# Kernel optimization log

Hardware: AMD Instinct MI355X
Metric: run time of the kernel (lower is better)

Reference implementation:

```python
import jax, jax.numpy as jnp
import numpy as np

WS = 7            # cubic window
HEADS = 6
DIM = 96          # attention channel dim (concat of two half-streams)
CH = 48           # per-stream channels (dim // 2)
HID = 384         # int(dim * mlp_ratio)
N = WS ** 3       # 343 tokens per window
EPS = 1e-5


def _rel_pos_index():
    c = np.stack(np.meshgrid(np.arange(WS), np.arange(WS), np.arange(WS), indexing='ij')).reshape(3, -1)
    rel = (c[:, :, None] - c[:, None, :]).transpose(1, 2, 0) + (WS - 1)
    rel[:, :, 0] *= (2 * WS - 1) * (2 * WS - 1)
    rel[:, :, 1] *= (2 * WS - 1)
    return rel.sum(-1)  # (N, N) int

RPI = jnp.asarray(_rel_pos_index())


def _ln(x, g, b):
    m = x.mean(-1, keepdims=True)
    v = ((x - m) ** 2).mean(-1, keepdims=True)
    return (x - m) * jax.lax.rsqrt(v + EPS) * g + b


def _win_part(x):
    B, H, W, T, C = x.shape
    x = x.reshape(B, H // WS, WS, W // WS, WS, T // WS, WS, C)
    return x.transpose(0, 1, 3, 5, 2, 4, 6, 7).reshape(-1, WS, WS, WS, C)


def _win_rev(w, B, H, W, T):
    C = w.shape[-1]
    x = w.reshape(B, H // WS, W // WS, T // WS, WS, WS, WS, C)
    return x.transpose(0, 1, 4, 2, 5, 3, 6, 7).reshape(B, H, W, T, C)


def _chessboard(wa, wb, gd, gh, gw):
    C = wa.shape[-1]
    a = wa.reshape(gd, gh, gw, WS, WS, WS, C)
    b = wb.reshape(gd, gh, gw, WS, WS, WS, C)
    i = jnp.arange(gd)[:, None, None]
    j = jnp.arange(gh)[None, :, None]
    k = jnp.arange(gw)[None, None, :]
    m = (((i + j + k) % 2) == 0)[..., None, None, None, None]
    return (jnp.where(m, a, b).reshape(-1, WS, WS, WS, C),
            jnp.where(m, b, a).reshape(-1, WS, WS, WS, C))


def _attn(x, mask, rpb, qkv_w, qkv_b, proj_w, proj_b):
    B_, n, C = x.shape
    hd = C // HEADS
    qkv = (x @ qkv_w + qkv_b).reshape(B_, n, 3, HEADS, hd).transpose(2, 0, 3, 1, 4)
    q, k, v = qkv[0] * (hd ** -0.5), qkv[1], qkv[2]
    att = jnp.einsum('bhnd,bhmd->bhnm', q, k)
    att = att + rpb[RPI].transpose(2, 0, 1)[None]   # relative position bias gather
    att = att + mask[:, None]                        # shift mask; B_ == nW since B == 1
    att = jax.nn.softmax(att, axis=-1)
    out = jnp.einsum('bhnm,bhmd->bhnd', att, v).transpose(0, 2, 1, 3).reshape(B_, n, C)
    return out @ proj_w + proj_b


def _mlp(x, w1, b1, w2, b2):
    return jax.nn.gelu(x @ w1 + b1, approximate=False) @ w2 + b2


def _forward(x_a, x_b, mask_matrix, n1a_g, n1a_b, n1b_g, n1b_b,
             rpb_a, qkvw_a, qkvb_a, projw_a, projb_a,
             rpb_b, qkvw_b, qkvb_b, projw_b, projb_b,
             n2a_g, n2a_b, n2b_g, n2b_b,
             fc1w_a, fc1b_a, fc2w_a, fc2b_a, fc1w_b, fc1b_b, fc2w_b, fc2b_b,
             gw1, gw2, gb2, H, W, T):
    B, L, _ = x_a.shape
    sa0, sb0 = x_a, x_b
    a = _ln(x_a, n1a_g, n1a_b).reshape(B, H, W, T, CH)
    b = _ln(x_b, n1b_g, n1b_b).reshape(B, H, W, T, CH)
    # chessboard cross-stream shuffle of windows (shifted-window branch)
    ca, cb = _chessboard(_win_part(a), _win_part(b), H // WS, W // WS, T // WS)
    a_cr = _win_rev(ca, B, H, W, T)
    b_cr = _win_rev(cb, B, H, W, T)
    neg, pos, dims = (-3, -3, -3), (3, 3, 3), (1, 2, 3)
    sa, sb = jnp.roll(a, neg, dims), jnp.roll(b, neg, dims)
    sac, sbc = jnp.roll(a_cr, neg, dims), jnp.roll(b_cr, neg, dims)
    xa_w = _win_part(jnp.concatenate([sa, sbc], -1)).reshape(-1, N, DIM)
    xb_w = _win_part(jnp.concatenate([sb, sac], -1)).reshape(-1, N, DIM)
    oa = _attn(xa_w, mask_matrix, rpb_a, qkvw_a, qkvb_a, projw_a, projb_a)
    ob = _attn(xb_w, mask_matrix, rpb_b, qkvw_b, qkvb_b, projw_b, projb_b)
    oa = jnp.roll(_win_rev(oa.reshape(-1, WS, WS, WS, DIM), B, H, W, T), pos, dims)[..., :CH].reshape(B, L, CH)
    ob = jnp.roll(_win_rev(ob.reshape(-1, WS, WS, WS, DIM), B, H, W, T), pos, dims)[..., :CH].reshape(B, L, CH)
    x_a = sa0 + oa
    x_b = sb0 + ob
    x_a = x_a + _mlp(_ln(x_a, n2a_g, n2a_b), fc1w_a, fc1b_a, fc2w_a, fc2b_a)
    x_b = x_b + _mlp(_ln(x_b, n2b_g, n2b_b), fc1w_b, fc1b_b, fc2w_b, fc2b_b)
    g = jax.nn.sigmoid(jnp.maximum(x_a.mean(1) @ gw1, 0.0) @ gw2 + gb2)[:, :, None]  # (B,1,1)
    x_a = x_a + g * x_b
    return x_a, x_b


def setup_inputs():
    key = jax.random.key(0)
    ks = iter(jax.random.split(key, 24))
    H = W = T = 35
    L = H * W * T
    nW = (H // WS) * (W // WS) * (T // WS)
    p = lambda shape: jax.random.normal(next(ks), shape, jnp.float32) * 0.02
    d = {
        'x_a': jax.random.normal(next(ks), (1, L, CH), jnp.float32),
        'x_b': jax.random.normal(next(ks), (1, L, CH), jnp.float32),
        'mask_matrix': jax.random.normal(next(ks), (nW, N, N), jnp.float32),
        'n1a_g': jnp.ones((CH,), jnp.float32), 'n1a_b': jnp.zeros((CH,), jnp.float32),
        'n1b_g': jnp.ones((CH,), jnp.float32), 'n1b_b': jnp.zeros((CH,), jnp.float32),
        'rpb_a': p(((2 * WS - 1) ** 3, HEADS)),
        'qkvw_a': p((DIM, 3 * DIM)), 'qkvb_a': jnp.zeros((3 * DIM,), jnp.float32),
        'projw_a': p((DIM, DIM)), 'projb_a': jnp.zeros((DIM,), jnp.float32),
        'rpb_b': p(((2 * WS - 1) ** 3, HEADS)),
        'qkvw_b': p((DIM, 3 * DIM)), 'qkvb_b': jnp.zeros((3 * DIM,), jnp.float32),
        'projw_b': p((DIM, DIM)), 'projb_b': jnp.zeros((DIM,), jnp.float32),
        'n2a_g': jnp.ones((CH,), jnp.float32), 'n2a_b': jnp.zeros((CH,), jnp.float32),
        'n2b_g': jnp.ones((CH,), jnp.float32), 'n2b_b': jnp.zeros((CH,), jnp.float32),
        'fc1w_a': p((CH, HID)), 'fc1b_a': jnp.zeros((HID,), jnp.float32),
        'fc2w_a': p((HID, CH)), 'fc2b_a': jnp.zeros((CH,), jnp.float32),
        'fc1w_b': p((CH, HID)), 'fc1b_b': jnp.zeros((HID,), jnp.float32),
        'fc2w_b': p((HID, CH)), 'fc2b_b': jnp.zeros((CH,), jnp.float32),
        'gw1': p((CH, CH // 4)), 'gw2': p((CH // 4, 1)),
        'gb2': jnp.full((1,), -2.0, jnp.float32),
        'H': H, 'W': W, 'T': T,
    }
    return d


def reference(x_a, x_b, mask_matrix, n1a_g, n1a_b, n1b_g, n1b_b,
              rpb_a, qkvw_a, qkvb_a, projw_a, projb_a,
              rpb_b, qkvw_b, qkvb_b, projw_b, projb_b,
              n2a_g, n2a_b, n2b_g, n2b_b,
              fc1w_a, fc1b_a, fc2w_a, fc2b_a, fc1w_b, fc1b_b, fc2w_b, fc2b_b,
              gw1, gw2, gb2, H, W, T):
    return _forward(x_a, x_b, mask_matrix, n1a_g, n1a_b, n1b_g, n1b_b,
                    rpb_a, qkvw_a, qkvb_a, projw_a, projb_a,
                    rpb_b, qkvw_b, qkvb_b, projw_b, projb_b,
                    n2a_g, n2a_b, n2b_g, n2b_b,
                    fc1w_a, fc1b_a, fc2w_a, fc2b_a, fc1w_b, fc1b_b, fc2w_b, fc2b_b,
                    gw1, gw2, gb2, H, W, T)
```

## Files before the change

### kernel.cpp

```cpp
#include <hip/hip_runtime.h>
#include <hip/hip_fp16.h>

#define LQ    42875
#define NTOK  343
#define X1SZ  2058000

#define OFF_MEAN 0
#define OFF_QKV  36928
#define OFF_WF   12500000
#define OFF_RPB  12600000
#define QKV_BYTES_NEEDED 56100000ull

typedef _Float16 f16x8 __attribute__((ext_vector_type(8)));
typedef float f32x4 __attribute__((ext_vector_type(4)));
union B128 { uint4 u; f16x8 h; _Float16 e[8]; };

__device__ __forceinline__ int src_index(int w, int i, int& par) {
  int gi = w / 25, gj = (w / 5) % 5, gk = w % 5;
  int ph = i / 49, pw = (i / 7) % 7, pt = i % 7;
  int hs = gi * 7 + ph + 3; if (hs >= 35) hs -= 35;
  int wd = gj * 7 + pw + 3; if (wd >= 35) wd -= 35;
  int td = gk * 7 + pt + 3; if (td >= 35) td -= 35;
  par = ((hs / 7) + (wd / 7) + (td / 7)) & 1;
  return (hs * 35 + wd) * 35 + td;
}

__global__ __launch_bounds__(64) void k_init(float* __restrict__ ws) {
  if (threadIdx.x < 49) ws[threadIdx.x] = 0.f;
}

__global__ __launch_bounds__(256) void k_pack(
    const float* __restrict__ w1a, const float* __restrict__ w1b,
    const float* __restrict__ w2a, const float* __restrict__ w2b,
    const float* __restrict__ qwa, const float* __restrict__ qwb,
    float* __restrict__ ws) {
  int idx = blockIdx.x * 256 + threadIdx.x;
  if (idx >= 17664) return;
  uint4* WFB = (uint4*)(ws + OFF_WF);
  unsigned short h[8];
  uint4* dst;
  if (idx < 10752) {
    int s = idx / 5376, r = idx - s * 5376;
    uint4* WF = WFB + (size_t)s * 5376;
    if (r < 3072) {
      int jn = r / 128, t = r - jn * 128, kk = t / 64, lane = t - kk * 64;
      int q = lane >> 4, n = lane & 15;
      const float* w1 = s ? w1b : w1a;
      int j = jn * 16 + n;
#pragma unroll
      for (int e = 0; e < 8; e++) {
        int k = kk * 32 + q * 8 + e;
        float v = (k < 48) ? w1[k * 384 + j] : 0.f;
        h[e] = __half_as_ushort(__float2half(v));
      }
    } else {
      int rr = r - 3072;
      int kt = rr / 192, t = rr - kt * 192, cn = t / 64, lane = t - cn * 64;
      int q = lane >> 4, n = lane & 15;
      const float* w2 = s ? w2b : w2a;
      int c = cn * 16 + n;
#pragma unroll
      for (int e = 0; e < 8; e++) {
        int j = kt * 32 + q * 8 + e;
        h[e] = __half_as_ushort(__float2half(w2[j * 48 + c]));
      }
    }
    dst = WF + r;
  } else {
    int idx2 = idx - 10752;
    int s = idx2 / 3456, r = idx2 - s * 3456;
    int jn = r / 192, t = r - jn * 192, kk = t / 64, lane = t - kk * 64;
    int q = lane >> 4, n = lane & 15;
    const float* qw = s ? qwb : qwa;
    int j = jn * 16 + n;
#pragma unroll
    for (int e = 0; e < 8; e++) {
      int k = kk * 32 + q * 8 + e;
      h[e] = __half_as_ushort(__float2half(qw[k * 288 + j]));
    }
    dst = WFB + 10752 + (size_t)s * 3456 + r;
  }
  uint4 u;
  u.x = (unsigned)h[0] | ((unsigned)h[1] << 16);
  u.y = (unsigned)h[2] | ((unsigned)h[3] << 16);
  u.z = (unsigned)h[4] | ((unsigned)h[5] << 16);
  u.w = (unsigned)h[6] | ((unsigned)h[7] << 16);
  *dst = u;
}

__global__ __launch_bounds__(256) void k_rpb(
    const float* __restrict__ rpa, const float* __restrict__ rpbp,
    float* __restrict__ ws) {
  int sh = blockIdx.y;
  int s = sh / 6, h = sh - s * 6;
  int idx = blockIdx.x * 256 + threadIdx.x;
  if (idx >= 117649) return;
  int ir = idx / 343, j = idx - ir * 343;
  int bi = (ir / 49) * 169 + ((ir / 7) % 7) * 13 + (ir % 7) + 1098;
  int bj = (j / 49) * 169 + ((j / 7) % 7) * 13 + (j % 7);
  const float* rp = s ? rpbp : rpa;
  ws[OFF_RPB + (size_t)sh * 117649 + idx] = rp[(bi - bj) * 6 + h];
}

__global__ __launch_bounds__(256) void k_qkv(
    const float* __restrict__ xa, const float* __restrict__ xb,
    const float* __restrict__ ga, const float* __restrict__ ba,
    const float* __restrict__ gb, const float* __restrict__ bb,
    const float* __restrict__ qba, const float* __restrict__ qbb,
    const float* __restrict__ ws, __half* __restrict__ qkvh) {
  __shared__ uint4 LDSB[2368];
  int s = blockIdx.z;
  int tid = threadIdx.x;
  int wid = tid >> 6, lane = tid & 63;
  int quad = lane >> 4, n15 = lane & 15;
  uint4* WR = LDSB + wid * 592;
  _Float16* th = (_Float16*)WR;
  int tbase = blockIdx.x * 64 + wid * 16;

  if (lane < 32) {
    int tt = lane & 15, which = lane >> 4;
    int t = tbase + tt;
    float v[48];
    bool wr = false, dup = false;
    if (t < LQ) {
      int w = t / 343, i = t - w * 343;
      int par; int src = src_index(w, i, par);
      const float* xr; const float* G; const float* B;
      bool doit;
      if (which == 0) { xr = (s ? xb : xa) + src * 48; G = s ? gb : ga; B = s ? bb : ba; doit = true; dup = (par == 1); }
      else            { xr = (s ? xa : xb) + src * 48; G = s ? ga : gb; B = s ? ba : bb; doit = (par == 0); }
      if (doit) {
        float sm = 0.f, sq = 0.f;
#pragma unroll
        for (int q4 = 0; q4 < 12; q4++) {
          float4 tv = ((const float4*)xr)[q4];
          v[4 * q4] = tv.x; v[4 * q4 + 1] = tv.y; v[4 * q4 + 2] = tv.z; v[4 * q4 + 3] = tv.w;
          sm += tv.x + tv.y + tv.z + tv.w;
          sq += tv.x * tv.x + tv.y * tv.y + tv.z * tv.z + tv.w * tv.w;
        }
        float m = sm * (1.f / 48.f);
        float r = rsqrtf(sq * (1.f / 48.f) - m * m + 1e-5f);
#pragma unroll
        for (int k = 0; k < 48; k++) v[k] = (v[k] - m) * r * G[k] + B[k];
        wr = true;
      }
    } else if (which == 0) {
#pragma unroll
      for (int k = 0; k < 48; k++) v[k] = 0.f;
      wr = true; dup = true;
    }
    if (wr) {
#pragma unroll
      for (int c6 = 0; c6 < 6; c6++) {
        unsigned short h[8];
#pragma unroll
        for (int e = 0; e < 8; e++) h[e] = __half_as_ushort(__float2half(v[c6 * 8 + e]));
        uint4 u;
        u.x = (unsigned)h[0] | ((unsigned)h[1] << 16);
        u.y = (unsigned)h[2] | ((unsigned)h[3] << 16);
        u.z = (unsigned)h[4] | ((unsigned)h[5] << 16);
        u.w = (unsigned)h[6] | ((unsigned)h[7] << 16);
        WR[(which * 6 + c6) * 16 + tt] = u;
        if (dup) WR[(6 + c6) * 16 + tt] = u;
      }
    }
  }

  B128 ax0, ax1, ax2;
  ax0.u = WR[(0 + quad) * 16 + n15];
  ax1.u = WR[(4 + quad) * 16 + n15];
  ax2.u = WR[(8 + quad) * 16 + n15];

  const uint4* QF = (const uint4*)(ws + OFF_WF) + 10752 + (size_t)s * 3456;
  const float* QB = s ? qbb : qba;
  const f32x4 ZC = {0.f, 0.f, 0.f, 0.f};

  for (int jn = 0; jn < 18; jn++) {
    B128 b0, b1, b2;
    b0.u = QF[(jn * 3 + 0) * 64 + lane];
    b1.u = QF[(jn * 3 + 1) * 64 + lane];
    b2.u = QF[(jn * 3 + 2) * 64 + lane];
    f32x4 c = __builtin_amdgcn_mfma_f32_16x16x32_f16(ax0.h, b0.h, ZC, 0, 0, 0);
    c = __builtin_amdgcn_mfma_f32_16x16x32_f16(ax1.h, b1.h, c, 0, 0, 0);
    c = __builtin_amdgcn_mfma_f32_16x16x32_f16(ax2.h, b2.h, c, 0, 0, 0);
    float bias = QB[jn * 16 + n15];
    float scale = (jn < 6) ? 0.25f : 1.0f;
#pragma unroll
    for (int r = 0; r < 4; r++)
      th[(quad * 4 + r) * 296 + jn * 16 + n15] = (_Float16)((c[r] + bias) * scale);
  }
  for (int e = lane; e < 576; e += 64) {
    int row = e / 36, cc = e - row * 36;
    int t = tbase + row;
    if (t < LQ)
      ((uint4*)qkvh)[(size_t)(s * LQ + t) * 36 + cc] = WR[row * 37 + cc];
  }
}

__global__ __launch_bounds__(256) void k_attn(
    const float* __restrict__ rpbmat,
    const float* __restrict__ mask, __half* __restrict__ qkvh) {
  int bid = blockIdx.x;
  int xcd = bid & 7, q8 = bid >> 3;
  int u = q8 / 12, inst = q8 - u * 12;
  int w = u * 8 + xcd;
  if (w >= 125) return;
  int s = inst & 1, h = inst >> 1;

  __shared__ uint4 FRAG[2368];
  uint4* Qf4 = FRAG;
  uint4* Kf4 = FRAG + 704;
  uint4* Vf4 = FRAG + 1408;
  uint4* Pb4 = FRAG + 2112;
  _Float16* Vfh = (_Float16*)(FRAG + 1408);
  _Float16* Pbh = (_Float16*)(FRAG + 2112);

  int tid = threadIdx.x;
  const uint4 Z4 = {0u, 0u, 0u, 0u};
  for (int e = tid; e < 2112; e += 256) FRAG[e] = Z4;
  __syncthreads();

  size_t wbase = (size_t)((s * 125 + w) * NTOK) * 288;
  for (int i = tid; i < NTOK; i += 256) {
    const uint4* row = (const uint4*)(qkvh + wbase + (size_t)i * 288) + (h * 2);
    uint4 q0 = row[0], q1 = row[1];
    uint4 k0 = row[12], k1 = row[13];
    B128 v0, v1; v0.u = row[24]; v1.u = row[25];
    int n = i & 15, it = i >> 4;
    Qf4[it * 32 + n] = q0;
    Qf4[it * 32 + 16 + n] = q1;
    Kf4[it * 32 + n] = k0;
    Kf4[it * 32 + 16 + n] = k1;
    int vbase = ((i >> 5) * 64 + ((i >> 3) & 3) * 16) * 8 + (i & 7);
#pragma unroll
    for (int d = 0; d < 8; d++) {
      Vfh[vbase + d * 8] = v0.e[d];
      Vfh[vbase + (d + 8) * 8] = v1.e[d];
    }
  }
  __syncthreads();

  int wid = tid >> 6, lane = tid & 63;
  int quad = lane >> 4, n15 = lane & 15;
  int jj = n15 & 7, hi = n15 >> 3;
  const f32x4 ZC = {0.f, 0.f, 0.f, 0.f};
  __half* obh = qkvh;
  const float* rbase = rpbmat + (size_t)(s * 6 + h) * 117649;

  int pA[4], pB[4];
#pragma unroll
  for (int r = 0; r < 4; r++) {
    int ra = hi * 16 + quad * 4 + r;
    int rb = (2 + hi) * 16 + quad * 4 + r;
    ra ^= (ra >> 3) & 7;
    rb ^= (rb >> 3) & 7;
    pA[r] = wid * 512 + ra * 8 + jj;
    pB[r] = wid * 512 + rb * 8 + jj;
  }
  int rdrow = wid * 64 + (lane ^ ((lane >> 3) & 7));

  for (int it = wid; it < 22; it += 4) {
    int i0 = it * 16;
    const float* mr[4]; const float* rr[4];
#pragma unroll
    for (int r = 0; r < 4; r++) {
      int ir = i0 + quad * 4 + r; if (ir > 342) ir = 342;
      mr[r] = mask + (size_t)(w * NTOK + ir) * NTOK;
      rr[r] = rbase + ir * NTOK;
    }
    B128 qbits; qbits.u = Qf4[it * 32 + ((quad & 1) << 4) + n15];
    if (quad >= 2) qbits.u = Z4;
    f32x4 acc = ZC;
    float ls[4] = {0.f, 0.f, 0.f, 0.f};

    float mcur[8], mnxt[8], rcur[8], rnxt[8];
    {
      int ja = n15, jb = n15 + 16;
#pragma unroll
      for (int r = 0; r < 4; r++) {
        mcur[r] = mr[r][ja]; mcur[4 + r] = mr[r][jb];
        rcur[r] = rr[r][ja]; rcur[4 + r] = rr[r][jb];
      }
    }
    for (int j32 = 0; j32 < 11; j32++) {
      if (j32 < 10) {
        int ja = (j32 + 1) * 32 + n15, jb = ja + 16;
        bool vb = jb < NTOK;
#pragma unroll
        for (int r = 0; r < 4; r++) {
          mnxt[r] = mr[r][ja];
          mnxt[4 + r] = vb ? mr[r][jb] : -1e30f;
          rnxt[r] = rr[r][ja];
          rnxt[4 + r] = vb ? rr[r][jb] : 0.f;
        }
      }
      B128 kb0, kb1;
      kb0.u = Kf4[(j32 * 2) * 32 + ((quad & 1) << 4) + n15];
      kb1.u = Kf4[(j32 * 2 + 1) * 32 + ((quad & 1) << 4) + n15];
      if (quad >= 2) { kb0.u = Z4; kb1.u = Z4; }
      f32x4 s0 = __builtin_amdgcn_mfma_f32_16x16x32_f16(qbits.h, kb0.h, ZC, 0, 0, 0);
      f32x4 s1 = __builtin_amdgcn_mfma_f32_16x16x32_f16(qbits.h, kb1.h, ZC, 0, 0, 0);
      float p0[4], p1[4];
#pragma unroll
      for (int r = 0; r < 4; r++) {
        p0[r] = __expf(s0[r] + mcur[r] + rcur[r]);
        p1[r] = __expf(s1[r] + mcur[4 + r] + rcur[4 + r]);
        ls[r] += p0[r] + p1[r];
      }
#pragma unroll
      for (int r = 0; r < 4; r++) {
        Pbh[pA[r]] = (_Float16)p0[r];
        Pbh[pB[r]] = (_Float16)p1[r];
      }
      B128 pb, vbits;
      pb.u = Pb4[rdrow];
      vbits.u = Vf4[j32 * 64 + lane];
      acc = __builtin_amdgcn_mfma_f32_16x16x32_f16(pb.h, vbits.h, acc, 0, 0, 0);
#pragma unroll
      for (int e = 0; e < 8; e++) { mcur[e] = mnxt[e]; rcur[e] = rnxt[e]; }
    }
#pragma unroll
    for (int r = 0; r < 4; r++) {
      float v = ls[r];
      v += __shfl_xor(v, 1); v += __shfl_xor(v, 2);
      v += __shfl_xor(v, 4); v += __shfl_xor(v, 8);
      int ir = i0 + quad * 4 + r;
      if (ir < 343)
        obh[wbase + (size_t)ir * 288 + h * 16 + n15] = __float2half(acc[r] * (1.f / v));
    }
  }
}

__global__ __launch_bounds__(384) void k_proj(
    const __half* __restrict__ qkvh,
    const float* __restrict__ xa0, const float* __restrict__ xb0,
    const float* __restrict__ pwa, const float* __restrict__ pba,
    const float* __restrict__ pwb, const float* __restrict__ pbb,
    float* __restrict__ out) {
  int sw = blockIdx.x; int s = sw / 125, w = sw - s * 125;
  int i = threadIdx.x;
  if (i >= NTOK) return;
  const float* Wt = s ? pwb : pwa;
  const float* Bi = s ? pbb : pba;
  const uint4* orow = (const uint4*)(qkvh + (size_t)((s * 125 + w) * NTOK + i) * 288);
  float acc[48];
#pragma unroll
  for (int c = 0; c < 48; c++) acc[c] = 0.f;
#pragma unroll
  for (int k8 = 0; k8 < 12; k8++) {
    B128 ov; ov.u = orow[k8];
#pragma unroll
    for (int e = 0; e < 8; e++) {
      float x = (float)ov.e[e];
      const float* wr = Wt + (k8 * 8 + e) * 96;
#pragma unroll
      for (int c = 0; c < 48; c++) acc[c] = fmaf(x, wr[c], acc[c]);
    }
  }
  int par; int src = src_index(w, i, par);
  const float* x0 = (s ? xb0 : xa0) + src * 48;
  float* dst = out + s * X1SZ + src * 48;
#pragma unroll
  for (int q = 0; q < 12; q++) {
    float4 xv = ((const float4*)x0)[q];
    float4 o;
    o.x = xv.x + acc[4 * q + 0] + Bi[4 * q + 0];
    o.y = xv.y + acc[4 * q + 1] + Bi[4 * q + 1];
    o.z = xv.z + acc[4 * q + 2] + Bi[4 * q + 2];
    o.w = xv.w + acc[4 * q + 3] + Bi[4 * q + 3];
    ((float4*)dst)[q] = o;
  }
}

__global__ __launch_bounds__(256) void k_mlp(
    const float* __restrict__ g2a, const float* __restrict__ b2a,
    const float* __restrict__ g2b, const float* __restrict__ b2b,
    const float* __restrict__ fb1a, const float* __restrict__ fb2a,
    const float* __restrict__ fb1b, const float* __restrict__ fb2b,
    float* __restrict__ out, float* __restrict__ ws) {
  __shared__ uint4 Xf[512];
  __shared__ uint4 tbu[320];
  __shared__ float red[48];
  int s = blockIdx.z;
  int tid = threadIdx.x;
  int wid = tid >> 6, lane = tid & 63;
  int quad = lane >> 4, n15 = lane & 15;
  if (tid < 48) red[tid] = 0.f;
  __syncthreads();

  const float* B1 = s ? fb1b : fb1a;
  const float* B2 = s ? fb2b : fb2a;
  const uint4* W1F = (const uint4*)(ws + OFF_WF) + (size_t)s * 5376;
  const uint4* W2F = W1F + 3072;
  int tbase = blockIdx.x * 64 + wid * 16;
  float* outs = out + (size_t)s * X1SZ;

  if (lane < 16) {
    int t = tbase + lane;
    float v[48];
    if (t < LQ) {
      const float* row = outs + (size_t)t * 48;
      float sm = 0.f, sq = 0.f;
#pragma unroll
      for (int q4 = 0; q4 < 12; q4++) {
        float4 tv = ((const float4*)row)[q4];
        v[4 * q4] = tv.x; v[4 * q4 + 1] = tv.y; v[4 * q4 + 2] = tv.z; v[4 * q4 + 3] = tv.w;
        sm += tv.x + tv.y + tv.z + tv.w;
        sq += tv.x * tv.x + tv.y * tv.y + tv.z * tv.z + tv.w * tv.w;
      }
      float m = sm * (1.f / 48.f);
      float r = rsqrtf(sq * (1.f / 48.f) - m * m + 1e-5f);
      const float* G = s ? g2b : g2a;
      const float* B = s ? b2b : b2a;
#pragma unroll
      for (int k = 0; k < 48; k++) v[k] = (v[k] - m) * r * G[k] + B[k];
    } else {
#pragma unroll
      for (int k = 0; k < 48; k++) v[k] = 0.f;
    }
#pragma unroll
    for (int kc = 0; kc < 8; kc++) {
      uint4 u = {0u, 0u, 0u, 0u};
      if (kc < 6) {
        unsigned short h[8];
#pragma unroll
        for (int e = 0; e < 8; e++) h[e] = __half_as_ushort(__float2half(v[kc * 8 + e]));
        u.x = (unsigned)h[0] | ((unsigned)h[1] << 16);
        u.y = (unsigned)h[2] | ((unsigned)h[3] << 16);
        u.z = (unsigned)h[4] | ((unsigned)h[5] << 16);
        u.w = (unsigned)h[6] | ((unsigned)h[7] << 16);
      }
      Xf[wid * 128 + kc * 16 + lane] = u;
    }
  }

  _Float16* mytb = (_Float16*)(tbu + wid * 80);
  const uint4* mytb4 = tbu + wid * 80;
  const f32x4 ZC = {0.f, 0.f, 0.f, 0.f};
  f32x4 oacc[3] = {ZC, ZC, ZC};
  B128 ax0, ax1;
  ax0.u = Xf[wid * 128 + quad * 16 + n15];
  ax1.u = Xf[wid * 128 + (4 + quad) * 16 + n15];

  for (int kt = 0; kt < 12; kt++) {
    int jn0 = kt * 2, jn1 = jn0 + 1;
    B128 w0, w1, w2, w3;
    w0.u = W1F[jn0 * 128 + lane];
    w1.u = W1F[jn0 * 128 + 64 + lane];
    w2.u = W1F[jn1 * 128 + lane];
    w3.u = W1F[jn1 * 128 + 64 + lane];
    f32x4 a0 = __builtin_amdgcn_mfma_f32_16x16x32_f16(ax0.h, w0.h, ZC, 0, 0, 0);
    a0 = __builtin_amdgcn_mfma_f32_16x16x32_f16(ax1.h, w1.h, a0, 0, 0, 0);
    f32x4 a1 = __builtin_amdgcn_mfma_f32_16x16x32_f16(ax0.h, w2.h, ZC, 0, 0, 0);
    a1 = __builtin_amdgcn_mfma_f32_16x16x32_f16(ax1.h, w3.h, a1, 0, 0, 0);
    float bz0 = B1[jn0 * 16 + n15], bz1 = B1[jn1 * 16 + n15];
#pragma unroll
    for (int r = 0; r < 4; r++) {
      float h0 = a0[r] + bz0;
      h0 = 0.5f * h0 * (1.f + erff(h0 * 0.70710678118654752f));
      float h1 = a1[r] + bz1;
      h1 = 0.5f * h1 * (1.f + erff(h1 * 0.70710678118654752f));
      int rowb = (quad * 4 + r) * 40;
      mytb[rowb + n15] = (_Float16)h0;
      mytb[rowb + 16 + n15] = (_Float16)h1;
    }
    B128 pa; pa.u = mytb4[n15 * 5 + quad];
    B128 c0, c1, c2;
    c0.u = W2F[kt * 192 + lane];
    c1.u = W2F[kt * 192 + 64 + lane];
    c2.u = W2F[kt * 192 + 128 + lane];
    oacc[0] = __builtin_amdgcn_mfma_f32_16x16x32_f16(pa.h, c0.h, oacc[0], 0, 0, 0);
    oacc[1] = __builtin_amdgcn_mfma_f32_16x16x32_f16(pa.h, c1.h, oacc[1], 0, 0, 0);
    oacc[2] = __builtin_amdgcn_mfma_f32_16x16x32_f16(pa.h, c2.h, oacc[2], 0, 0, 0);
  }

  float b2v[3];
#pragma unroll
  for (int cn = 0; cn < 3; cn++) b2v[cn] = B2[cn * 16 + n15];
  float gsum[3] = {0.f, 0.f, 0.f};
#pragma unroll
  for (int r = 0; r < 4; r++) {
    int t = tbase + quad * 4 + r;
    bool val = t < LQ;
    float* orow = outs + (size_t)(val ? t : 0) * 48;
#pragma unroll
    for (int cn = 0; cn < 3; cn++) {
      float fin = 0.f;
      if (val) {
        fin = orow[cn * 16 + n15] + oacc[cn][r] + b2v[cn];
        orow[cn * 16 + n15] = fin;
      }
      gsum[cn] += fin;
    }
  }
  if (s == 0) {
#pragma unroll
    for (int cn = 0; cn < 3; cn++) {
      float v = gsum[cn];
      v += __shfl_xor(v, 16); v += __shfl_xor(v, 32);
      if (quad == 0) atomicAdd(&red[cn * 16 + n15], v);
    }
  }
  __syncthreads();
  if (s == 0 && tid < 48) atomicAdd(ws + OFF_MEAN + tid, red[tid]);
}

__global__ __launch_bounds__(64) void k_gate(
    const float* __restrict__ ws_mean, const float* __restrict__ gw1,
    const float* __restrict__ gw2, const float* __restrict__ gb2,
    float* __restrict__ g) {
  int j = threadIdx.x;
  float t = 0.f;
  if (j < 12) {
    for (int c = 0; c < 48; c++)
      t = fmaf(ws_mean[c] * (1.f / (float)LQ), gw1[c * 12 + j], t);
    t = fmaxf(t, 0.f) * gw2[j];
  }
  for (int off = 32; off > 0; off >>= 1) t += __shfl_down(t, off);
  if (j == 0) *g = 1.f / (1.f + __expf(-(t + gb2[0])));
}

__global__ __launch_bounds__(256) void k_gadd(float* __restrict__ out,
                                              const float* __restrict__ g) {
  int i = blockIdx.x * 256 + threadIdx.x;
  if (i >= X1SZ / 4) return;
  float gv = *g;
  float4* a = (float4*)out;
  const float4* b = (const float4*)(out + X1SZ);
  float4 x = a[i], y = b[i];
  x.x = fmaf(gv, y.x, x.x);
  x.y = fmaf(gv, y.y, x.y);
  x.z = fmaf(gv, y.z, x.z);
  x.w = fmaf(gv, y.w, x.w);
  a[i] = x;
}

extern "C" void kernel_launch(void* const* d_in, const int* in_sizes, int n_in,
                              void* d_out, int out_size, void* d_ws, size_t ws_size,
                              hipStream_t stream) {
  const float* xa    = (const float*)d_in[0];
  const float* xb    = (const float*)d_in[1];
  const float* mask  = (const float*)d_in[2];
  const float* n1ag  = (const float*)d_in[3];
  const float* n1ab  = (const float*)d_in[4];
  const float* n1bg  = (const float*)d_in[5];
  const float* n1bb  = (const float*)d_in[6];
  const float* rpba  = (const float*)d_in[7];
  const float* qkvwa = (const float*)d_in[8];
  const float* qkvba = (const float*)d_in[9];
  const float* pwa   = (const float*)d_in[10];
  const float* pba   = (const float*)d_in[11];
  const float* rpbb  = (const float*)d_in[12];
  const float* qkvwb = (const float*)d_in[13];
  const float* qkvbb = (const float*)d_in[14];
  const float* pwb   = (const float*)d_in[15];
  const float* pbb   = (const float*)d_in[16];
  const float* n2ag  = (const float*)d_in[17];
  const float* n2ab  = (const float*)d_in[18];
  const float* n2bg  = (const float*)d_in[19];
  const float* n2bb  = (const float*)d_in[20];
  const float* w1a   = (const float*)d_in[21];
  const float* fb1a  = (const float*)d_in[22];
  const float* w2a   = (const float*)d_in[23];
  const float* fb2a  = (const float*)d_in[24];
  const float* w1b   = (const float*)d_in[25];
  const float* fb1b  = (const float*)d_in[26];
  const float* w2b   = (const float*)d_in[27];
  const float* fb2b  = (const float*)d_in[28];
  const float* gw1   = (const float*)d_in[29];
  const float* gw2   = (const float*)d_in[30];
  const float* gb2   = (const float*)d_in[31];
  float* ws  = (float*)d_ws;
  float* out = (float*)d_out;

  if (ws_size < QKV_BYTES_NEEDED) return;
  __half* qkvh = (__half*)(ws + OFF_QKV);

  hipLaunchKernelGGL(k_init, dim3(1), dim3(64), 0, stream, ws);
  hipLaunchKernelGGL(k_pack, dim3(69), dim3(256), 0, stream,
                     w1a, w1b, w2a, w2b, qkvwa, qkvwb, ws);
  hipLaunchKernelGGL(k_rpb, dim3(460, 12), dim3(256), 0, stream,
                     rpba, rpbb, ws);
  hipLaunchKernelGGL(k_qkv, dim3(670, 1, 2), dim3(256), 0, stream,
                     xa, xb, n1ag, n1ab, n1bg, n1bb,
                     qkvba, qkvbb, ws, qkvh);
  hipLaunchKernelGGL(k_attn, dim3(1536), dim3(256), 0, stream,
                     ws + OFF_RPB, mask, qkvh);
  hipLaunchKernelGGL(k_proj, dim3(250), dim3(384), 0, stream,
                     qkvh, xa, xb, pwa, pba, pwb, pbb, out);
  hipLaunchKernelGGL(k_mlp, dim3(670, 1, 2), dim3(256), 0, stream,
                     n2ag, n2ab, n2bg, n2bb,
                     fb1a, fb2a, fb1b, fb2b, out, ws);
  hipLaunchKernelGGL(k_gate, dim3(1), dim3(64), 0, stream,
                     ws + OFF_MEAN, gw1, gw2, gb2, ws + OFF_MEAN + 48);
  hipLaunchKernelGGL(k_gadd, dim3(2011), dim3(256), 0, stream,
                     out, ws + OFF_MEAN + 48);
}
```

Before: 458.8 us.

## Store rel-pos bias and mask in fp16, read Q from global in attention

Stores the relative-position bias matrix as fp16 and, when the workspace is large enough, adds a pass that converts the shift mask to fp16, so the attention kernel streams half the bytes for its bias and mask operands. Q fragments are now loaded directly from global memory instead of being staged in LDS, which shrinks shared memory per block and may raise occupancy. The cost is an extra full pass over the fp32 mask each call, which writes a large fp16 copy. Mask values such as large negatives lose precision or become infinite in fp16.

```diff
diff --git a/kernel.cpp b/kernel.cpp
--- a/kernel.cpp
+++ b/kernel.cpp
@@ -9,7 +9,10 @@
 #define OFF_QKV  36928
 #define OFF_WF   12500000
 #define OFF_RPB  12600000
+#define OFF_MASKH 13400000
+#define MASKH_ELEMS 14706125ull
 #define QKV_BYTES_NEEDED 56100000ull
+#define MASKH_BYTES_NEEDED 83100000ull
 
 typedef _Float16 f16x8 __attribute__((ext_vector_type(8)));
 typedef float f32x4 __attribute__((ext_vector_type(4)));
@@ -99,7 +102,21 @@
   int bi = (ir / 49) * 169 + ((ir / 7) % 7) * 13 + (ir % 7) + 1098;
   int bj = (j / 49) * 169 + ((j / 7) % 7) * 13 + (j % 7);
   const float* rp = s ? rpbp : rpa;
-  ws[OFF_RPB + (size_t)sh * 117649 + idx] = rp[(bi - bj) * 6 + h];
+  ((__half*)(ws + OFF_RPB))[(size_t)sh * 117649 + idx] =
+      __float2half(rp[(bi - bj) * 6 + h]);
+}
+
+__global__ __launch_bounds__(256) void k_maskh(
+    const float* __restrict__ mask, __half* __restrict__ mh) {
+  size_t i = ((size_t)blockIdx.x * 256 + threadIdx.x) * 4;
+  if (i + 4 <= MASKH_ELEMS) {
+    float4 v = *(const float4*)(mask + i);
+    __half2* d = (__half2*)(mh + i);
+    d[0] = __floats2half2_rn(v.x, v.y);
+    d[1] = __floats2half2_rn(v.z, v.w);
+  } else {
+    for (; i < MASKH_ELEMS; i++) mh[i] = __float2half(mask[i]);
+  }
 }
 
 __global__ __launch_bounds__(256) void k_qkv(
@@ -197,9 +214,10 @@
   }
 }
 
+template <typename MT>
 __global__ __launch_bounds__(256) void k_attn(
-    const float* __restrict__ rpbmat,
-    const float* __restrict__ mask, __half* __restrict__ qkvh) {
+    const __half* __restrict__ rpbmat,
+    const MT* __restrict__ mask, __half* __restrict__ qkvh) {
   int bid = blockIdx.x;
   int xcd = bid & 7, q8 = bid >> 3;
   int u = q8 / 12, inst = q8 - u * 12;
@@ -207,28 +225,24 @@
   if (w >= 125) return;
   int s = inst & 1, h = inst >> 1;
 
-  __shared__ uint4 FRAG[2368];
-  uint4* Qf4 = FRAG;
-  uint4* Kf4 = FRAG + 704;
-  uint4* Vf4 = FRAG + 1408;
-  uint4* Pb4 = FRAG + 2112;
-  _Float16* Vfh = (_Float16*)(FRAG + 1408);
-  _Float16* Pbh = (_Float16*)(FRAG + 2112);
+  __shared__ uint4 FRAG[1664];
+  uint4* Kf4 = FRAG;
+  uint4* Vf4 = FRAG + 704;
+  uint4* Pb4 = FRAG + 1408;
+  _Float16* Vfh = (_Float16*)(FRAG + 704);
+  _Float16* Pbh = (_Float16*)(FRAG + 1408);
 
   int tid = threadIdx.x;
   const uint4 Z4 = {0u, 0u, 0u, 0u};
-  for (int e = tid; e < 2112; e += 256) FRAG[e] = Z4;
+  for (int e = tid; e < 1408; e += 256) FRAG[e] = Z4;
   __syncthreads();
 
   size_t wbase = (size_t)((s * 125 + w) * NTOK) * 288;
   for (int i = tid; i < NTOK; i += 256) {
     const uint4* row = (const uint4*)(qkvh + wbase + (size_t)i * 288) + (h * 2);
-    uint4 q0 = row[0], q1 = row[1];
     uint4 k0 = row[12], k1 = row[13];
     B128 v0, v1; v0.u = row[24]; v1.u = row[25];
     int n = i & 15, it = i >> 4;
-    Qf4[it * 32 + n] = q0;
-    Qf4[it * 32 + 16 + n] = q1;
     Kf4[it * 32 + n] = k0;
     Kf4[it * 32 + 16 + n] = k1;
     int vbase = ((i >> 5) * 64 + ((i >> 3) & 3) * 16) * 8 + (i & 7);
@@ -245,7 +259,7 @@
   int jj = n15 & 7, hi = n15 >> 3;
   const f32x4 ZC = {0.f, 0.f, 0.f, 0.f};
   __half* obh = qkvh;
-  const float* rbase = rpbmat + (size_t)(s * 6 + h) * 117649;
+  const __half* rbase = rpbmat + (size_t)(s * 6 + h) * 117649;
 
   int pA[4], pB[4];
 #pragma unroll
@@ -261,15 +275,19 @@
 
   for (int it = wid; it < 22; it += 4) {
     int i0 = it * 16;
-    const float* mr[4]; const float* rr[4];
+    const MT* mr[4]; const __half* rr[4];
 #pragma unroll
     for (int r = 0; r < 4; r++) {
       int ir = i0 + quad * 4 + r; if (ir > 342) ir = 342;
       mr[r] = mask + (size_t)(w * NTOK + ir) * NTOK;
       rr[r] = rbase + ir * NTOK;
     }
-    B128 qbits; qbits.u = Qf4[it * 32 + ((quad & 1) << 4) + n15];
-    if (quad >= 2) qbits.u = Z4;
+    B128 qbits;
+    int qtok = i0 + n15;
+    if (quad < 2 && qtok < NTOK)
+      qbits.u = *((const uint4*)(qkvh + wbase + (size_t)qtok * 288) + h * 2 + (quad & 1));
+    else
+      qbits.u = Z4;
     f32x4 acc = ZC;
     float ls[4] = {0.f, 0.f, 0.f, 0.f};
 
@@ -278,8 +296,8 @@
       int ja = n15, jb = n15 + 16;
 #pragma unroll
       for (int r = 0; r < 4; r++) {
-        mcur[r] = mr[r][ja]; mcur[4 + r] = mr[r][jb];
-        rcur[r] = rr[r][ja]; rcur[4 + r] = rr[r][jb];
+        mcur[r] = (float)mr[r][ja]; mcur[4 + r] = (float)mr[r][jb];
+        rcur[r] = (float)rr[r][ja]; rcur[4 + r] = (float)rr[r][jb];
       }
     }
     for (int j32 = 0; j32 < 11; j32++) {
@@ -288,10 +306,10 @@
         bool vb = jb < NTOK;
 #pragma unroll
         for (int r = 0; r < 4; r++) {
-          mnxt[r] = mr[r][ja];
-          mnxt[4 + r] = vb ? mr[r][jb] : -1e30f;
-          rnxt[r] = rr[r][ja];
-          rnxt[4 + r] = vb ? rr[r][jb] : 0.f;
+          mnxt[r] = (float)mr[r][ja];
+          mnxt[4 + r] = vb ? (float)mr[r][jb] : -1e30f;
+          rnxt[r] = (float)rr[r][ja];
+          rnxt[4 + r] = vb ? (float)rr[r][jb] : 0.f;
         }
       }
       B128 kb0, kb1;
@@ -575,17 +593,26 @@
 
   if (ws_size < QKV_BYTES_NEEDED) return;
   __half* qkvh = (__half*)(ws + OFF_QKV);
+  bool bigmask = ws_size >= MASKH_BYTES_NEEDED;
 
   hipLaunchKernelGGL(k_init, dim3(1), dim3(64), 0, stream, ws);
   hipLaunchKernelGGL(k_pack, dim3(69), dim3(256), 0, stream,
                      w1a, w1b, w2a, w2b, qkvwa, qkvwb, ws);
   hipLaunchKernelGGL(k_rpb, dim3(460, 12), dim3(256), 0, stream,
                      rpba, rpbb, ws);
+  if (bigmask)
+    hipLaunchKernelGGL(k_maskh, dim3(14362), dim3(256), 0, stream,
+                       mask, (__half*)(ws + OFF_MASKH));
   hipLaunchKernelGGL(k_qkv, dim3(670, 1, 2), dim3(256), 0, stream,
                      xa, xb, n1ag, n1ab, n1bg, n1bb,
                      qkvba, qkvbb, ws, qkvh);
-  hipLaunchKernelGGL(k_attn, dim3(1536), dim3(256), 0, stream,
-                     ws + OFF_RPB, mask, qkvh);
+  if (bigmask)
+    hipLaunchKernelGGL((k_attn<__half>), dim3(1536), dim3(256), 0, stream,
+                       (const __half*)(ws + OFF_RPB),
+                       (const __half*)(ws + OFF_MASKH), qkvh);
+  else
+    hipLaunchKernelGGL((k_attn<float>), dim3(1536), dim3(256), 0, stream,
+                       (const __half*)(ws + OFF_RPB), mask, qkvh);
   hipLaunchKernelGGL(k_proj, dim3(250), dim3(384), 0, stream,
                      qkvh, xa, xb, pwa, pba, pwb, pbb, out);
   hipLaunchKernelGGL(k_mlp, dim3(670, 1, 2), dim3(256), 0, stream,
```

Measured after the change: 438.2 us. 1.05x faster.
